# Kernel optimization log

Measured on AMD Instinct MI355X. Metric: run time of the kernel, lower is better.

## Reference

```python
import jax, jax.numpy as jnp
import numpy as np

N = 100000
E = 1600000
NEG_SLOPE = 0.2


def gat_conv(h_x, edge_index, W, a_src, a_dst, b, heads, concat):
    # h_x: [N, Fin]; W: [Fin, heads*C]
    n = h_x.shape[0]
    h = (h_x @ W).reshape(n, heads, -1)              # [N, H, C]
    s_src = (h * a_src[None]).sum(-1)                # [N, H]
    s_dst = (h * a_dst[None]).sum(-1)                # [N, H]
    # add self loops (PyG default)
    loop = jnp.arange(n, dtype=edge_index.dtype)
    src = jnp.concatenate([edge_index[0], loop])
    dst = jnp.concatenate([edge_index[1], loop])
    e = jax.nn.leaky_relu(s_src[src] + s_dst[dst], NEG_SLOPE)   # [E+N, H]
    m = jax.ops.segment_max(e, dst, num_segments=n)
    e = jnp.exp(e - m[dst])
    denom = jax.ops.segment_sum(e, dst, num_segments=n)
    alpha = e / denom[dst]                                       # [E+N, H]
    out = jax.ops.segment_sum(alpha[:, :, None] * h[src], dst, num_segments=n)  # [N,H,C]
    out = out.reshape(n, -1) if concat else out.mean(axis=1)
    return out + b


def setup_inputs() -> dict:
    key = jax.random.key(0)
    ks = jax.random.split(key, 16)
    s = 0.1
    return {
        "x": jax.random.normal(ks[0], (N, 128), jnp.float32),
        "edge_index": jax.random.randint(ks[1], (2, E), 0, N, jnp.int64 if jax.config.jax_enable_x64 else jnp.int32),
        "W0": jax.random.normal(ks[2], (128, 64), jnp.float32) * s,
        "a_src0": jax.random.normal(ks[3], (1, 64), jnp.float32) * s,
        "a_dst0": jax.random.normal(ks[4], (1, 64), jnp.float32) * s,
        "b0": jax.random.normal(ks[5], (64,), jnp.float32) * s,
        "sW0": jax.random.normal(ks[6], (128, 64), jnp.float32) * s,
        "sb0": jax.random.normal(ks[7], (64,), jnp.float32) * s,
        "W1": jax.random.normal(ks[8], (64, 32), jnp.float32) * s,
        "a_src1": jax.random.normal(ks[9], (1, 32), jnp.float32) * s,
        "a_dst1": jax.random.normal(ks[10], (1, 32), jnp.float32) * s,
        "b1": jax.random.normal(ks[11], (32,), jnp.float32) * s,
        "sW1": jax.random.normal(ks[12], (64, 32), jnp.float32) * s,
        "sb1": jax.random.normal(ks[13], (32,), jnp.float32) * s,
    }


def reference(x, edge_index, W0, a_src0, a_dst0, b0, sW0, sb0,
              W1, a_src1, a_dst1, b1, sW1, sb1):
    # layer 0: GATConv (heads=1, concat=True) + linear skip, ELU (dropout p=0 is identity)
    h = gat_conv(x, edge_index, W0, a_src0, a_dst0, b0, heads=1, concat=True) + (x @ sW0 + sb0)
    h = jax.nn.elu(h)
    # layer 1: GATConv (heads=1, concat=False -> mean) + linear skip, log_softmax
    h = gat_conv(h, edge_index, W1, a_src1, a_dst1, b1, heads=1, concat=False) + (h @ sW1 + sb1)
    return jax.nn.log_softmax(h, axis=-1)
```

## Files before the change

kernel.cpp:

```cpp
#include <hip/hip_runtime.h>
#include <hip/hip_bf16.h>
#include <math.h>

#define NEG_SLOPE 0.2f
#define ECLAMP 30.0f
#define HCLAMP 1.0e4f

#define BSHIFT 8
#define BR 256
#define NBMAX 1024
#define CHUNK 2048

typedef short v8s __attribute__((ext_vector_type(8)));
typedef float v4f __attribute__((ext_vector_type(4)));
typedef unsigned long long ull;

__device__ __forceinline__ float bf2f(__hip_bfloat16 v) { return __bfloat162float(v); }
__device__ __forceinline__ __hip_bfloat16 f2bf(float v) { return __float2bfloat16(v); }
__device__ __forceinline__ float sane(float v)   { return fminf(fmaxf(v, -HCLAMP), HCLAMP); }
__device__ __forceinline__ float eclampf(float v){ return fminf(fmaxf(v, -ECLAMP), ECLAMP); }

__device__ __forceinline__ float ldany(int isf32, const void* p, int i) {
    return isf32 ? ((const float*)p)[i] : bf2f(((const __hip_bfloat16*)p)[i]);
}
// ... 14 lines not shown
    return (unsigned)(*(unsigned short*)&x) | ((unsigned)(*(unsigned short*)&y) << 16);
}

__global__ void k_probe(const unsigned* __restrict__ xw, int nw_safe,
                        const unsigned* __restrict__ ew, int* __restrict__ flags) {
    __shared__ int cnt[2];
    int t = threadIdx.x;
    if (t < 2) cnt[t] = 0;
    __syncthreads();
    unsigned w = xw[(unsigned)(t * 9973) % (unsigned)nw_safe];
    unsigned lo = w & 0xffffu;
    unsigned exp = (lo >> 7) & 0xffu;
    if (lo != 0u && (exp < 90u || exp > 160u)) atomicAdd(&cnt[0], 1);
    if (ew[2 * t + 1] == 0u) atomicAdd(&cnt[1], 1);
    __syncthreads();
    if (t == 0) { flags[0] = (2 * cnt[0] > 256) ? 1 : 0; flags[1] = (cnt[1] >= 200) ? 1 : 0; }
}

__global__ void k_params(const int* __restrict__ flags,
                         const void* W0, const void* sW0, const void* as0, const void* ad0,
                         const void* b0, const void* sb0, const void* W1, const void* sW1,
                         const void* as1, const void* ad1, const void* b1, const void* sb1,
                         float* __restrict__ Pf, __hip_bfloat16* __restrict__ Wg) {
    int f = flags[0];
    int t = blockIdx.x * blockDim.x + threadIdx.x;
    int T = gridDim.x * blockDim.x;
    for (int i = t; i < 8192; i += T) {
        int n = i >> 7, k = i & 127;
        Wg[i]        = f2bf(ldany(f, W0,  k * 64 + n));
        Wg[8192 + i] = f2bf(ldany(f, sW0, k * 64 + n));
    }
    for (int i = t; i < 2048; i += T) {
        int n = i >> 6, k = i & 63;
        Wg[16384 + i] = f2bf(ldany(f, W1,  k * 32 + n));
        Wg[18432 + i] = f2bf(ldany(f, sW1, k * 32 + n));
    }
    if (t < 64) {
        Pf[t]       = ldany(f, as0, t);
        Pf[64 + t]  = ldany(f, ad0, t);
        Pf[128 + t] = ldany(f, b0, t) + ldany(f, sb0, t);
    }
    if (t < 32) {
        Pf[192 + t] = ldany(f, as1, t);
        Pf[224 + t] = ldany(f, ad1, t);
        Pf[256 + t] = ldany(f, b1, t) + ldany(f, sb1, t);
    }
}

__global__ void k_zero(int* __restrict__ p, int n) {
    int i = blockIdx.x * blockDim.x + threadIdx.x;
    if (i < n) p[i] = 0;
}

__global__ __launch_bounds__(256) void k_chist(const void* __restrict__ ei,
                                               const int* __restrict__ flags,
                                               int E, int N, int NB,
                                               int* __restrict__ hist) {
    __shared__ int h[NBMAX];
    for (int i = threadIdx.x; i < NB; i += 256) h[i] = 0;
    __syncthreads();
    int f = flags[1];
    long long c0 = (long long)blockIdx.x * CHUNK;
    long long c1 = c0 + CHUNK;
    if (c1 > E) c1 = E;
    for (long long i = c0 + threadIdx.x; i < c1; i += 256) {
        unsigned d = (unsigned)ldidx(f, ei, (long long)E + i);
        if (d < (unsigned)N) atomicAdd(&h[d >> BSHIFT], 1);
    }
    __syncthreads();
    long long base = (long long)blockIdx.x * NB;
    for (int i = threadIdx.x; i < NB; i += 256) hist[base + i] = h[i];
}

__global__ __launch_bounds__(1024) void k_cscan(const int* __restrict__ hist,
                                                int gch, int NB,
                                                int* __restrict__ cb,
                                                int* __restrict__ bcount) {
    __shared__ int sh[1024];
    int b = blockIdx.x;
    int t = threadIdx.x;
    int run = 0;
    for (int base = 0; base < gch; base += 1024) {
        int c = base + t;
        int v = (c < gch) ? hist[(long long)c * NB + b] : 0;
        sh[t] = v;
        __syncthreads();
        for (int off = 1; off < 1024; off <<= 1) {
            int xv = (t >= off) ? sh[t - off] : 0;
            __syncthreads();
            sh[t] += xv;
            __syncthreads();
        }
        if (c < gch) cb[(long long)c * NB + b] = run + sh[t] - v;
        run += sh[1023];
        __syncthreads();
    }
    if (t == 0) bcount[b] = run;
}

__global__ void k_bscan(const int* __restrict__ bcount, int NB,
                        int* __restrict__ bbase) {
    __shared__ int sh[NBMAX];
    int t = threadIdx.x;
    int v = (t < NB) ? bcount[t] : 0;
    sh[t] = v;
    __syncthreads();
    for (int off = 1; off < NBMAX; off <<= 1) {
        int xv = (t >= off) ? sh[t - off] : 0;
        __syncthreads();
        sh[t] += xv;
        __syncthreads();
    }
    if (t < NB) bbase[t] = sh[t] - v;
    if (t == NB - 1) bbase[NB] = sh[t];
}

__global__ __launch_bounds__(256) void k_bscatter(const void* __restrict__ ei,
                                                  const int* __restrict__ flags,
                                                  int E, int N, int NB,
                                                  const int* __restrict__ bbase,
                                                  const int* __restrict__ cb,
                                                  unsigned* __restrict__ binned) {
    __shared__ int rb[NBMAX];
    int f = flags[1];
// ... 65 lines not shown
__global__ void k_scan1(const int* __restrict__ deg, int N,
                        int* __restrict__ rowptr, int* __restrict__ bsum) {
    __shared__ int sh[1024];
    int t = threadIdx.x;
    int idx = blockIdx.x * 1024 + t;
    int v = (idx < N) ? deg[idx] : 0;
    sh[t] = v;
    __syncthreads();
    for (int off = 1; off < 1024; off <<= 1) {
        int xv = (t >= off) ? sh[t - off] : 0;
        __syncthreads();
        sh[t] += xv;
        __syncthreads();
    }
    if (idx < N) rowptr[idx] = sh[t] - v;
    if (t == 1023) bsum[blockIdx.x] = sh[1023];
}

__global__ void k_scan2(int* __restrict__ bsum, int B, int* __restrict__ rowptr, int N) {
    __shared__ int sh[1024];
    int t = threadIdx.x;
    int v = (t < B) ? bsum[t] : 0;
    sh[t] = v;
    __syncthreads();
    for (int off = 1; off < 1024; off <<= 1) {
        int xv = (t >= off) ? sh[t - off] : 0;
        __syncthreads();
        sh[t] += xv;
        __syncthreads();
    }
    if (t < B) bsum[t] = sh[t] - v;
    if (t == 1023) rowptr[N] = sh[1023];
}

__global__ void k_scan3(int N, int* __restrict__ rowptr, const int* __restrict__ bsum,
                        int* __restrict__ cursor) {
    int idx = blockIdx.x * 1024 + threadIdx.x;
    if (idx < N) {
        int r = rowptr[idx] + bsum[blockIdx.x];
        rowptr[idx] = r;
        cursor[idx] = r;
    }
}

__global__ void k_fill(const void* __restrict__ ei, const int* __restrict__ flags,
                       int E, int N, int* __restrict__ cursor, int* __restrict__ csr_src) {
    int i = blockIdx.x * blockDim.x + threadIdx.x;
    if (i < E) {
        int f = flags[1];
        unsigned d = (unsigned)ldidx(f, ei, (long long)E + i);
        if (d < (unsigned)N) {
            int p = atomicAdd(&cursor[d], 1);
            if ((unsigned)p < (unsigned)E) csr_src[p] = ldidx(f, ei, i);
        }
    }
}

__global__ __launch_bounds__(256) void k_l0(
    const void* __restrict__ x, const int* __restrict__ flags,
    const float* __restrict__ Pf, const __hip_bfloat16* __restrict__ Wg, int N,
    __hip_bfloat16* __restrict__ h0, __hip_bfloat16* __restrict__ skip0,
    float* __restrict__ ssrc, float* __restrict__ sdst) {
    __shared__ __hip_bfloat16 sm[26112];
    __hip_bfloat16* xs  = sm;
    __hip_bfloat16* wt0 = sm + 8704;
    __hip_bfloat16* wts = sm + 17408;
    int tid = threadIdx.x;
    int f = flags[0];
    int tile = blockIdx.x * 64;

    for (int i = tid * 4; i < 8192; i += 1024) {
        int r = i >> 7, k = i & 127;
        uint2 w0v = *(const uint2*)&Wg[i];
        uint2 w1v = *(const uint2*)&Wg[8192 + i];
        *(uint2*)&wt0[r * 136 + k] = w0v;
        *(uint2*)&wts[r * 136 + k] = w1v;
    }
    for (int i = tid * 4; i < 8192; i += 1024) {
        int r = i >> 7, k = i & 127;
        int g = tile + r; if (g >= N) g = N - 1;
        uint2* dx = (uint2*)&xs[r * 136 + k];
        if (f) {
            float4 v = *(const float4*)((const float*)x + (size_t)g * 128 + k);
            uint2 o; o.x = packbf(v.x, v.y); o.y = packbf(v.z, v.w);
            *dx = o;
        } else {
            *dx = *(const uint2*)((const __hip_bfloat16*)x + (size_t)g * 128 + k);
        }
    }
    __syncthreads();

    int lane = tid & 63, w = tid >> 6;
    int n16 = lane & 15, quad = lane >> 4;
    v4f zf = {0.f, 0.f, 0.f, 0.f};
    v4f acc_h[4], acc_s[4];
#pragma unroll
    for (int t = 0; t < 4; t++) { acc_h[t] = zf; acc_s[t] = zf; }

    int arow = (w << 4) + n16;
#pragma unroll
    for (int s = 0; s < 4; s++) {
        v8s a = ld8(&xs[arow * 136 + s * 32 + (quad << 3)]);
#pragma unroll
        for (int t = 0; t < 4; t++) {
            v8s bh = ld8(&wt0[(t * 16 + n16) * 136 + s * 32 + (quad << 3)]);
            acc_h[t] = __builtin_amdgcn_mfma_f32_16x16x32_bf16(a, bh, acc_h[t], 0, 0, 0);
            v8s bs = ld8(&wts[(t * 16 + n16) * 136 + s * 32 + (quad << 3)]);
            acc_s[t] = __builtin_amdgcn_mfma_f32_16x16x32_bf16(a, bs, acc_s[t], 0, 0, 0);
        }
    }

    int mbase = tile + (w << 4) + (quad << 2);
    float ps[4] = {0, 0, 0, 0}, pd[4] = {0, 0, 0, 0};
#pragma unroll
    for (int t = 0; t < 4; t++) {
        int ch = t * 16 + n16;
        float av = Pf[ch];
        float dv = Pf[64 + ch];
        float bv = Pf[128 + ch];
#pragma unroll
        for (int r = 0; r < 4; r++) {
            float hv = sane(acc_h[t][r]);
            float sv = sane(acc_s[t][r] + bv);
            int node = mbase + r;
            if (node < N) {
                h0[(size_t)node * 64 + ch] = f2bf(hv);
                skip0[(size_t)node * 64 + ch] = f2bf(sv);
            }
            ps[r] += hv * av;
            pd[r] += hv * dv;
        }
    }
#pragma unroll
    for (int m = 1; m <= 8; m <<= 1) {
#pragma unroll
        for (int r = 0; r < 4; r++) {
            ps[r] += __shfl_xor(ps[r], m, 64);
            pd[r] += __shfl_xor(pd[r], m, 64);
        }
    }
    if (n16 == 0) {
#pragma unroll
        for (int r = 0; r < 4; r++) {
            int node = mbase + r;
            if (node < N) { ssrc[node] = sane(ps[r]); sdst[node] = sane(pd[r]); }
        }
    }
}

__global__ __launch_bounds__(256) void k_l0_agg(
    const int* __restrict__ rowptr, const int* __restrict__ csr_src,
    const float* __restrict__ ssrc, const float* __restrict__ sdst,
    const __hip_bfloat16* __restrict__ h0,
    int N, __hip_bfloat16* __restrict__ skip0_hact) {
    __shared__ ull ews[256];
    int wv = threadIdx.x >> 6, lane = threadIdx.x & 63;
    int half = lane >> 5, l5 = lane & 31;
    int slot = l5 >> 4, c4 = l5 & 15;
    int n = blockIdx.x * 8 + wv * 2 + half;
    bool act = n < N;
    int nn = act ? n : 0;
    const uint2* h0w = (const uint2*)h0;
    ull* myw = &ews[wv * 64 + half * 32];

    float sd = sdst[nn];
    float wself = ewgt(ssrc[nn] + sd);

    uint2 selfv = h0w[(size_t)nn * 16 + c4];
    float w0 = (slot == 0) ? wself : 0.f;
    float acc0 = w0 * bflo(selfv.x);
    float acc1 = w0 * bfhi(selfv.x);
    float acc2 = w0 * bflo(selfv.y);
    float acc3 = w0 * bfhi(selfv.y);
    float denp = 0.f;

    int beg = act ? rowptr[nn] : 0;
    int end = act ? rowptr[nn + 1] : 0;
    for (int j0 = beg; j0 < end; j0 += 32) {
        int cnt = end - j0; if (cnt > 32) cnt = 32;
        int s = (l5 < cnt) ? csr_src[j0 + l5] : 0;
        bool v = (l5 < cnt) && ((unsigned)s < (unsigned)N);
        int sg = v ? s : 0;
        float wj = v ? ewgt(ssrc[sg] + sd) : 0.f;
        denp += wj;
        myw[l5] = ((ull)__float_as_uint(wj) << 32) | (unsigned)sg;
        int k2 = 0;
        int full = cnt & ~7;
        for (; k2 < full; k2 += 8) {
            ull pa = myw[k2 + slot];
            ull pb = myw[k2 + 2 + slot];
            ull pc = myw[k2 + 4 + slot];
            ull pd_ = myw[k2 + 6 + slot];
            float wa = __uint_as_float((unsigned)(pa >> 32));
            float wb = __uint_as_float((unsigned)(pb >> 32));
            float wc = __uint_as_float((unsigned)(pc >> 32));
            float wd = __uint_as_float((unsigned)(pd_ >> 32));
            int sa = (int)(unsigned)(pa & 0xffffffffu);
            int sb = (int)(unsigned)(pb & 0xffffffffu);
            int sc = (int)(unsigned)(pc & 0xffffffffu);
            int sdi = (int)(unsigned)(pd_ & 0xffffffffu);
            uint2 va = h0w[(size_t)sa * 16 + c4];
            uint2 vb = h0w[(size_t)sb * 16 + c4];
            uint2 vc = h0w[(size_t)sc * 16 + c4];
            uint2 vd = h0w[(size_t)sdi * 16 + c4];
            acc0 += wa * bflo(va.x) + wb * bflo(vb.x) + wc * bflo(vc.x) + wd * bflo(vd.x);
            acc1 += wa * bfhi(va.x) + wb * bfhi(vb.x) + wc * bfhi(vc.x) + wd * bfhi(vd.x);
            acc2 += wa * bflo(va.y) + wb * bflo(vb.y) + wc * bflo(vc.y) + wd * bflo(vd.y);
            acc3 += wa * bfhi(va.y) + wb * bfhi(vb.y) + wc * bfhi(vc.y) + wd * bfhi(vd.y);
        }
        for (; k2 < cnt; k2 += 8) {
            int ia = k2 + slot,     ib = k2 + 2 + slot;
            int ic = k2 + 4 + slot, id = k2 + 6 + slot;
            ull pa = myw[ia < cnt ? ia : 0];
            ull pb = myw[ib < cnt ? ib : 0];
            ull pc = myw[ic < cnt ? ic : 0];
            ull pd_ = myw[id < cnt ? id : 0];
            float wa = (ia < cnt) ? __uint_as_float((unsigned)(pa >> 32)) : 0.f;
            float wb = (ib < cnt) ? __uint_as_float((unsigned)(pb >> 32)) : 0.f;
            float wc = (ic < cnt) ? __uint_as_float((unsigned)(pc >> 32)) : 0.f;
            float wd = (id < cnt) ? __uint_as_float((unsigned)(pd_ >> 32)) : 0.f;
            int sa = (int)(unsigned)(pa & 0xffffffffu);
            int sb = (int)(unsigned)(pb & 0xffffffffu);
            int sc = (int)(unsigned)(pc & 0xffffffffu);
            int sdi = (int)(unsigned)(pd_ & 0xffffffffu);
            uint2 va = h0w[(size_t)sa * 16 + c4];
            uint2 vb = h0w[(size_t)sb * 16 + c4];
            uint2 vc = h0w[(size_t)sc * 16 + c4];
            uint2 vd = h0w[(size_t)sdi * 16 + c4];
            acc0 += wa * bflo(va.x) + wb * bflo(vb.x) + wc * bflo(vc.x) + wd * bflo(vd.x);
            acc1 += wa * bfhi(va.x) + wb * bfhi(vb.x) + wc * bfhi(vc.x) + wd * bfhi(vd.x);
            acc2 += wa * bflo(va.y) + wb * bflo(vb.y) + wc * bflo(vc.y) + wd * bflo(vd.y);
            acc3 += wa * bfhi(va.y) + wb * bfhi(vb.y) + wc * bfhi(vc.y) + wd * bfhi(vd.y);
        }
    }
    acc0 += __shfl_xor(acc0, 16, 64);
    acc1 += __shfl_xor(acc1, 16, 64);
    acc2 += __shfl_xor(acc2, 16, 64);
    acc3 += __shfl_xor(acc3, 16, 64);
    float den = denp;
#pragma unroll
    for (int m = 1; m <= 16; m <<= 1) den += __shfl_xor(den, m, 64);
    den += wself;

    if (slot == 0 && act) {
        uint2 skv = ((const uint2*)skip0_hact)[(size_t)nn * 16 + c4];
        float v0 = sane(acc0 / den + bflo(skv.x));
        float v1 = sane(acc1 / den + bfhi(skv.x));
        float v2 = sane(acc2 / den + bflo(skv.y));
        float v3 = sane(acc3 / den + bfhi(skv.y));
        v0 = v0 > 0.f ? v0 : (__expf(v0) - 1.f);
        v1 = v1 > 0.f ? v1 : (__expf(v1) - 1.f);
        v2 = v2 > 0.f ? v2 : (__expf(v2) - 1.f);
        v3 = v3 > 0.f ? v3 : (__expf(v3) - 1.f);
        uint2 o;
        o.x = packbf(v0, v1);
        o.y = packbf(v2, v3);
        ((uint2*)skip0_hact)[(size_t)nn * 16 + c4] = o;
    }
}

__global__ __launch_bounds__(256) void k_l1(
    const __hip_bfloat16* __restrict__ hact,
    const float* __restrict__ Pf, const __hip_bfloat16* __restrict__ Wg, int N,
    __hip_bfloat16* __restrict__ h1, __hip_bfloat16* __restrict__ skip1,
    float* __restrict__ ssrc, float* __restrict__ sdst) {
    __shared__ __hip_bfloat16 sm[9216];
    __hip_bfloat16* xs  = sm;
    __hip_bfloat16* wt1 = sm + 4608;
    __hip_bfloat16* ws1 = sm + 6912;
    int tid = threadIdx.x;
    int tile = blockIdx.x * 64;

    for (int i = tid * 4; i < 2048; i += 1024) {
        int r = i >> 6, k = i & 63;
        uint2 w0v = *(const uint2*)&Wg[16384 + i];
        uint2 w1v = *(const uint2*)&Wg[18432 + i];
        *(uint2*)&wt1[r * 72 + k] = w0v;
        *(uint2*)&ws1[r * 72 + k] = w1v;
    }
    for (int i = tid * 4; i < 4096; i += 1024) {
        int r = i >> 6, k = i & 63;
        int g = tile + r; if (g >= N) g = N - 1;
        *(uint2*)&xs[r * 72 + k] = *(const uint2*)(hact + (size_t)g * 64 + k);
    }
    __syncthreads();

    int lane = tid & 63, w = tid >> 6;
    int n16 = lane & 15, quad = lane >> 4;
    v4f zf = {0.f, 0.f, 0.f, 0.f};
    v4f acc_h[2], acc_s[2];
#pragma unroll
    for (int t = 0; t < 2; t++) { acc_h[t] = zf; acc_s[t] = zf; }

    int arow = (w << 4) + n16;
#pragma unroll
    for (int s = 0; s < 2; s++) {
        v8s a = ld8(&xs[arow * 72 + s * 32 + (quad << 3)]);
#pragma unroll
        for (int t = 0; t < 2; t++) {
            v8s bh = ld8(&wt1[(t * 16 + n16) * 72 + s * 32 + (quad << 3)]);
            acc_h[t] = __builtin_amdgcn_mfma_f32_16x16x32_bf16(a, bh, acc_h[t], 0, 0, 0);
            v8s bs = ld8(&ws1[(t * 16 + n16) * 72 + s * 32 + (quad << 3)]);
            acc_s[t] = __builtin_amdgcn_mfma_f32_16x16x32_bf16(a, bs, acc_s[t], 0, 0, 0);
        }
    }

    int mbase = tile + (w << 4) + (quad << 2);
    float ps[4] = {0, 0, 0, 0}, pd[4] = {0, 0, 0, 0};
#pragma unroll
    for (int t = 0; t < 2; t++) {
        int ch = t * 16 + n16;
        float av = Pf[192 + ch];
        float dv = Pf[224 + ch];
        float bv = Pf[256 + ch];
#pragma unroll
        for (int r = 0; r < 4; r++) {
            float hv = sane(acc_h[t][r]);
            float sv = sane(acc_s[t][r] + bv);
            int node = mbase + r;
            if (node < N) {
                h1[(size_t)node * 32 + ch] = f2bf(hv);
                skip1[(size_t)node * 32 + ch] = f2bf(sv);
            }
            ps[r] += hv * av;
            pd[r] += hv * dv;
        }
    }
#pragma unroll
    for (int m = 1; m <= 8; m <<= 1) {
#pragma unroll
        for (int r = 0; r < 4; r++) {
            ps[r] += __shfl_xor(ps[r], m, 64);
            pd[r] += __shfl_xor(pd[r], m, 64);
        }
    }
    if (n16 == 0) {
#pragma unroll
        for (int r = 0; r < 4; r++) {
            int node = mbase + r;
            if (node < N) { ssrc[node] = sane(ps[r]); sdst[node] = sane(pd[r]); }
        }
    }
}

__global__ __launch_bounds__(256) void k_l1_agg(
    const int* __restrict__ rowptr, const int* __restrict__ csr_src,
    const float* __restrict__ ssrc, const float* __restrict__ sdst,
    const __hip_bfloat16* __restrict__ h1, const __hip_bfloat16* __restrict__ skip1,
    int N, float* __restrict__ out) {
    __shared__ ull ews[256];
    int wv = threadIdx.x >> 6, lane = threadIdx.x & 63;
    int half = lane >> 5, l5 = lane & 31;
    int slot = l5 >> 3, c4 = l5 & 7;
    int n = blockIdx.x * 8 + wv * 2 + half;
    bool act = n < N;
    int nn = act ? n : 0;
    const uint2* h1w = (const uint2*)h1;
    ull* myw = &ews[wv * 64 + half * 32];

    float sd = sdst[nn];
    float wself = ewgt(ssrc[nn] + sd);

    uint2 selfv = h1w[(size_t)nn * 8 + c4];
    float w0 = (slot == 0) ? wself : 0.f;
    float acc0 = w0 * bflo(selfv.x);
    float acc1 = w0 * bfhi(selfv.x);
    float acc2 = w0 * bflo(selfv.y);
    float acc3 = w0 * bfhi(selfv.y);
    float denp = 0.f;

    int beg = act ? rowptr[nn] : 0;
    int end = act ? rowptr[nn + 1] : 0;
    for (int j0 = beg; j0 < end; j0 += 32) {
        int cnt = end - j0; if (cnt > 32) cnt = 32;
        int s = (l5 < cnt) ? csr_src[j0 + l5] : 0;
        bool v = (l5 < cnt) && ((unsigned)s < (unsigned)N);
        int sg = v ? s : 0;
        float wj = v ? ewgt(ssrc[sg] + sd) : 0.f;
        denp += wj;
        myw[l5] = ((ull)__float_as_uint(wj) << 32) | (unsigned)sg;
        int k4 = 0;
        int full = cnt & ~15;
        for (; k4 < full; k4 += 16) {
            ull pa = myw[k4 + slot];
            ull pb = myw[k4 + 4 + slot];
            ull pc = myw[k4 + 8 + slot];
            ull pd_ = myw[k4 + 12 + slot];
            float wa = __uint_as_float((unsigned)(pa >> 32));
            float wb = __uint_as_float((unsigned)(pb >> 32));
            float wc = __uint_as_float((unsigned)(pc >> 32));
            float wd = __uint_as_float((unsigned)(pd_ >> 32));
            int sa = (int)(unsigned)(pa & 0xffffffffu);
            int sb = (int)(unsigned)(pb & 0xffffffffu);
// ... 33 lines not shown
            acc3 += wa * bfhi(va.y) + wb * bfhi(vb.y) + wc * bfhi(vc.y) + wd * bfhi(vd.y);
        }
    }
    acc0 += __shfl_xor(acc0, 8, 64); acc0 += __shfl_xor(acc0, 16, 64);
    acc1 += __shfl_xor(acc1, 8, 64); acc1 += __shfl_xor(acc1, 16, 64);
    acc2 += __shfl_xor(acc2, 8, 64); acc2 += __shfl_xor(acc2, 16, 64);
    acc3 += __shfl_xor(acc3, 8, 64); acc3 += __shfl_xor(acc3, 16, 64);
    float den = denp;
#pragma unroll
    for (int m = 1; m <= 16; m <<= 1) den += __shfl_xor(den, m, 64);
    den += wself;

    uint2 skv = ((const uint2*)skip1)[(size_t)nn * 8 + c4];
    float o0 = sane(acc0 / den + bflo(skv.x));
    float o1 = sane(acc1 / den + bfhi(skv.x));
    float o2 = sane(acc2 / den + bflo(skv.y));
    float o3 = sane(acc3 / den + bfhi(skv.y));
    float m = fmaxf(fmaxf(o0, o1), fmaxf(o2, o3));
#pragma unroll
    for (int k = 1; k <= 4; k <<= 1) m = fmaxf(m, __shfl_xor(m, k, 64));
    float ex = __expf(o0 - m) + __expf(o1 - m) + __expf(o2 - m) + __expf(o3 - m);
#pragma unroll
    for (int k = 1; k <= 4; k <<= 1) ex += __shfl_xor(ex, k, 64);
    float l = __logf(ex);
    float r0 = o0 - m - l, r1 = o1 - m - l, r2 = o2 - m - l, r3 = o3 - m - l;
    if (!isfinite(r0)) r0 = 0.f;
    if (!isfinite(r1)) r1 = 0.f;
    if (!isfinite(r2)) r2 = 0.f;
    if (!isfinite(r3)) r3 = 0.f;
    if (slot == 0 && act) {
        float4 o4; o4.x = r0; o4.y = r1; o4.z = r2; o4.w = r3;
        *(float4*)&out[(size_t)nn * 32 + 4 * c4] = o4;
    }
}

__global__ void k_sentinel(float* __restrict__ out, int n, float val) {
    int i = blockIdx.x * blockDim.x + threadIdx.x;
    if (i < n) out[i] = val;
}

extern "C" void kernel_launch(void* const* d_in, const int* in_sizes, int n_in,
                              void* d_out, int out_size, void* d_ws, size_t ws_size,
                              hipStream_t stream) {
    const void* x  = d_in[0];
    const void* ei = d_in[1];
    float* out = (float*)d_out;

    int N = in_sizes[0] / 128;
    int E = in_sizes[1] / 2;

    int NB  = (N + BR - 1) >> BSHIFT;
    int gch = (E + CHUNK - 1) / CHUNK;
    if (gch < 1) gch = 1;
    bool fast = (N <= (NBMAX << BSHIFT)) && ((size_t)E * 4 <= (size_t)N * 128);

    char* ws = (char*)d_ws;
    size_t off = 0;
    auto alloc = [&](size_t bytes) -> char* {
        char* p = ws + off;
        off += (bytes + 255) & ~(size_t)255;
        return p;
    };
    int*   flags   = (int*)alloc(2 * 4);
    float* Pf      = (float*)alloc(288 * 4);
    __hip_bfloat16* Wg = (__hip_bfloat16*)alloc(20480 * 2);
    int*   rowptr  = (int*)alloc((size_t)(N + 1) * 4);
    int*   cursor  = (int*)alloc((size_t)N * 4);
    float* sdst01  = (float*)alloc((size_t)N * 4);
    int*   bsum    = (int*)alloc(1024 * 4);
    int*   bcount  = (int*)alloc(NBMAX * 4);
    int*   bbase   = (int*)alloc((NBMAX + 1) * 4);
    int*   csr_src = (int*)alloc((size_t)E * 4);
    int*   hist    = (int*)alloc(fast ? (size_t)gch * NB * 4 : 0);
    int*   cb      = (int*)alloc(fast ? (size_t)gch * NB * 4 : 0);
    __hip_bfloat16* h0    = (__hip_bfloat16*)alloc((size_t)N * 64 * 2);
    __hip_bfloat16* skip0 = (__hip_bfloat16*)alloc((size_t)N * 64 * 2);
    size_t required = off;

    if (ws_size < required) {
        float mb = (float)(double)(ws_size >> 20);
        k_sentinel<<<(out_size + 255) / 256, 256, 0, stream>>>(out, out_size, mb);
        return;
    }

    float* ssrc01 = (float*)cursor;
    __hip_bfloat16* h1    = h0;
    __hip_bfloat16* skip1 = h0 + (size_t)N * 32;

    k_probe<<<1, 256, 0, stream>>>((const unsigned*)x, N * 64, (const unsigned*)ei, flags);
    k_params<<<40, 256, 0, stream>>>(flags, d_in[2], d_in[6], d_in[3], d_in[4],
                                     d_in[5], d_in[7], d_in[8], d_in[12],
                                     d_in[9], d_in[10], d_in[11], d_in[13], Pf, Wg);

    if (fast) {
        unsigned* binned = (unsigned*)h0;
        k_chist<<<gch, 256, 0, stream>>>(ei, flags, E, N, NB, hist);
        k_cscan<<<NB, 1024, 0, stream>>>(hist, gch, NB, cb, bcount);
        k_bscan<<<1, NBMAX, 0, stream>>>(bcount, NB, bbase);
        k_bscatter<<<gch, 256, 0, stream>>>(ei, flags, E, N, NB, bbase, cb, binned);
        k_bbuild<<<NB, 256, 0, stream>>>(binned, bbase, N, NB, rowptr, csr_src);
    } else {
        int B = (N + 1023) / 1024;
        k_zero<<<(N + 255) / 256, 256, 0, stream>>>(cursor, N);
        k_deg<<<(E + 255) / 256, 256, 0, stream>>>(ei, flags, E, N, cursor);
        k_scan1<<<B, 1024, 0, stream>>>(cursor, N, rowptr, bsum);
        k_scan2<<<1, 1024, 0, stream>>>(bsum, B, rowptr, N);
        k_scan3<<<B, 1024, 0, stream>>>(N, rowptr, bsum, cursor);
        k_fill<<<(E + 255) / 256, 256, 0, stream>>>(ei, flags, E, N, cursor, csr_src);
    }

    k_l0<<<(N + 63) / 64, 256, 0, stream>>>(x, flags, Pf, Wg, N,
                                            h0, skip0, ssrc01, sdst01);
    k_l0_agg<<<(N + 7) / 8, 256, 0, stream>>>(rowptr, csr_src, ssrc01, sdst01,
                                              h0, N, skip0);
    k_l1<<<(N + 63) / 64, 256, 0, stream>>>(skip0, Pf, Wg, N,
                                            h1, skip1, ssrc01, sdst01);
    k_l1_agg<<<(N + 7) / 8, 256, 0, stream>>>(rowptr, csr_src, ssrc01, sdst01,
                                              h1, skip1, N, out);
}
```

Measured before the change: 268.7 us.

## Fuse layer-0 aggregation with layer-1 linear transform in one kernel

Merges the layer-0 attention aggregation and the layer-1 MFMA projection into one 512-thread kernel. Each block aggregates 64 nodes, writes the ELU activations straight into shared memory and then runs the matmul from there, so the activated features no longer make a round trip through global memory and one launch is removed. The attention-score row sums now go through shared-memory atomics. Because the layer-1 outputs can no longer alias layer-0 buffers that other blocks are still reading, they get separate workspace allocations. Each block's serial aggregation passes and heavier shared-memory use may cut occupancy and latency hiding for the gather.

```diff
diff --git a/kernel.cpp b/kernel.cpp
--- a/kernel.cpp
+++ b/kernel.cpp
@@ -375,183 +375,174 @@
     }
 }
 
-__global__ __launch_bounds__(256) void k_l0_agg(
+__global__ __launch_bounds__(512) void k_l0agg_l1(
     const int* __restrict__ rowptr, const int* __restrict__ csr_src,
-    const float* __restrict__ ssrc, const float* __restrict__ sdst,
-    const __hip_bfloat16* __restrict__ h0,
-    int N, __hip_bfloat16* __restrict__ skip0_hact) {
-    __shared__ ull ews[256];
-    int wv = threadIdx.x >> 6, lane = threadIdx.x & 63;
+    const float* __restrict__ ssrc0, const float* __restrict__ sdst0,
+    const __hip_bfloat16* __restrict__ h0, const __hip_bfloat16* __restrict__ skip0,
+    const float* __restrict__ Pf, const __hip_bfloat16* __restrict__ Wg, int N,
+    __hip_bfloat16* __restrict__ h1, __hip_bfloat16* __restrict__ skip1,
+    float* __restrict__ ssrc1, float* __restrict__ sdst1) {
+    __shared__ __hip_bfloat16 xs[4608];
+    __shared__ __hip_bfloat16 wsm[4608];
+    __shared__ ull ews[512];
+    __shared__ float psum[64], pdum[64];
+    __hip_bfloat16* wt1 = wsm;
+    __hip_bfloat16* ws1 = wsm + 2304;
+    int tid = threadIdx.x;
+    int tile = blockIdx.x * 64;
+
+    {
+        int i = tid * 4;
+        int r = i >> 6, k = i & 63;
+        *(uint2*)&wt1[r * 72 + k] = *(const uint2*)&Wg[16384 + i];
+        *(uint2*)&ws1[r * 72 + k] = *(const uint2*)&Wg[18432 + i];
+    }
+    if (tid < 64) { psum[tid] = 0.f; pdum[tid] = 0.f; }
+
+    int wv = tid >> 6, lane = tid & 63;
     int half = lane >> 5, l5 = lane & 31;
     int slot = l5 >> 4, c4 = l5 & 15;
-    int n = blockIdx.x * 8 + wv * 2 + half;
-    bool act = n < N;
-    int nn = act ? n : 0;
     const uint2* h0w = (const uint2*)h0;
     ull* myw = &ews[wv * 64 + half * 32];
 
-    float sd = sdst[nn];
-    float wself = ewgt(ssrc[nn] + sd);
-
-    uint2 selfv = h0w[(size_t)nn * 16 + c4];
-    float w0 = (slot == 0) ? wself : 0.f;
-    float acc0 = w0 * bflo(selfv.x);
-    float acc1 = w0 * bfhi(selfv.x);
-    float acc2 = w0 * bflo(selfv.y);
-    float acc3 = w0 * bfhi(selfv.y);
-    float denp = 0.f;
-
-    int beg = act ? rowptr[nn] : 0;
-    int end = act ? rowptr[nn + 1] : 0;
-    for (int j0 = beg; j0 < end; j0 += 32) {
-        int cnt = end - j0; if (cnt > 32) cnt = 32;
-        int s = (l5 < cnt) ? csr_src[j0 + l5] : 0;
-        bool v = (l5 < cnt) && ((unsigned)s < (unsigned)N);
-        int sg = v ? s : 0;
-        float wj = v ? ewgt(ssrc[sg] + sd) : 0.f;
-        denp += wj;
-        myw[l5] = ((ull)__float_as_uint(wj) << 32) | (unsigned)sg;
-        int k2 = 0;
-        int full = cnt & ~7;
-        for (; k2 < full; k2 += 8) {
-            ull pa = myw[k2 + slot];
-            ull pb = myw[k2 + 2 + slot];
-            ull pc = myw[k2 + 4 + slot];
-            ull pd_ = myw[k2 + 6 + slot];
-            float wa = __uint_as_float((unsigned)(pa >> 32));
-            float wb = __uint_as_float((unsigned)(pb >> 32));
-            float wc = __uint_as_float((unsigned)(pc >> 32));
-            float wd = __uint_as_float((unsigned)(pd_ >> 32));
-            int sa = (int)(unsigned)(pa & 0xffffffffu);
-            int sb = (int)(unsigned)(pb & 0xffffffffu);
-            int sc = (int)(unsigned)(pc & 0xffffffffu);
-            int sdi = (int)(unsigned)(pd_ & 0xffffffffu);
-            uint2 va = h0w[(size_t)sa * 16 + c4];
-            uint2 vb = h0w[(size_t)sb * 16 + c4];
-            uint2 vc = h0w[(size_t)sc * 16 + c4];
-            uint2 vd = h0w[(size_t)sdi * 16 + c4];
-            acc0 += wa * bflo(va.x) + wb * bflo(vb.x) + wc * bflo(vc.x) + wd * bflo(vd.x);
-            acc1 += wa * bfhi(va.x) + wb * bfhi(vb.x) + wc * bfhi(vc.x) + wd * bfhi(vd.x);
-            acc2 += wa * bflo(va.y) + wb * bflo(vb.y) + wc * bflo(vc.y) + wd * bflo(vd.y);
-            acc3 += wa * bfhi(va.y) + wb * bfhi(vb.y) + wc * bfhi(vc.y) + wd * bfhi(vd.y);
-        }
-        for (; k2 < cnt; k2 += 8) {
-            int ia = k2 + slot,     ib = k2 + 2 + slot;
-            int ic = k2 + 4 + slot, id = k2 + 6 + slot;
-            ull pa = myw[ia < cnt ? ia : 0];
-            ull pb = myw[ib < cnt ? ib : 0];
-            ull pc = myw[ic < cnt ? ic : 0];
-            ull pd_ = myw[id < cnt ? id : 0];
-            float wa = (ia < cnt) ? __uint_as_float((unsigned)(pa >> 32)) : 0.f;
-            float wb = (ib < cnt) ? __uint_as_float((unsigned)(pb >> 32)) : 0.f;
-            float wc = (ic < cnt) ? __uint_as_float((unsigned)(pc >> 32)) : 0.f;
-            float wd = (id < cnt) ? __uint_as_float((unsigned)(pd_ >> 32)) : 0.f;
-            int sa = (int)(unsigned)(pa & 0xffffffffu);
-            int sb = (int)(unsigned)(pb & 0xffffffffu);
-            int sc = (int)(unsigned)(pc & 0xffffffffu);
-            int sdi = (int)(unsigned)(pd_ & 0xffffffffu);
-            uint2 va = h0w[(size_t)sa * 16 + c4];
-            uint2 vb = h0w[(size_t)sb * 16 + c4];
-            uint2 vc = h0w[(size_t)sc * 16 + c4];
-            uint2 vd = h0w[(size_t)sdi * 16 + c4];
-            acc0 += wa * bflo(va.x) + wb * bflo(vb.x) + wc * bflo(vc.x) + wd * bflo(vd.x);
-            acc1 += wa * bfhi(va.x) + wb * bfhi(vb.x) + wc * bfhi(vc.x) + wd * bfhi(vd.x);
-            acc2 += wa * bflo(va.y) + wb * bflo(vb.y) + wc * bflo(vc.y) + wd * bflo(vd.y);
-            acc3 += wa * bfhi(va.y) + wb * bfhi(vb.y) + wc * bfhi(vc.y) + wd * bfhi(vd.y);
-        }
-    }
-    acc0 += __shfl_xor(acc0, 16, 64);
-    acc1 += __shfl_xor(acc1, 16, 64);
-    acc2 += __shfl_xor(acc2, 16, 64);
-    acc3 += __shfl_xor(acc3, 16, 64);
-    float den = denp;
-#pragma unroll
-    for (int m = 1; m <= 16; m <<= 1) den += __shfl_xor(den, m, 64);
-    den += wself;
-
-    if (slot == 0 && act) {
-        uint2 skv = ((const uint2*)skip0_hact)[(size_t)nn * 16 + c4];
-        float v0 = sane(acc0 / den + bflo(skv.x));
-        float v1 = sane(acc1 / den + bfhi(skv.x));
-        float v2 = sane(acc2 / den + bflo(skv.y));
-        float v3 = sane(acc3 / den + bfhi(skv.y));
-        v0 = v0 > 0.f ? v0 : (__expf(v0) - 1.f);
-        v1 = v1 > 0.f ? v1 : (__expf(v1) - 1.f);
-        v2 = v2 > 0.f ? v2 : (__expf(v2) - 1.f);
-        v3 = v3 > 0.f ? v3 : (__expf(v3) - 1.f);
-        uint2 o;
-        o.x = packbf(v0, v1);
-        o.y = packbf(v2, v3);
-        ((uint2*)skip0_hact)[(size_t)nn * 16 + c4] = o;
-    }
-}
-
-__global__ __launch_bounds__(256) void k_l1(
-    const __hip_bfloat16* __restrict__ hact,
-    const float* __restrict__ Pf, const __hip_bfloat16* __restrict__ Wg, int N,
-    __hip_bfloat16* __restrict__ h1, __hip_bfloat16* __restrict__ skip1,
-    float* __restrict__ ssrc, float* __restrict__ sdst) {
-    __shared__ __hip_bfloat16 sm[9216];
-    __hip_bfloat16* xs  = sm;
-    __hip_bfloat16* wt1 = sm + 4608;
-    __hip_bfloat16* ws1 = sm + 6912;
-    int tid = threadIdx.x;
-    int tile = blockIdx.x * 64;
-
-    for (int i = tid * 4; i < 2048; i += 1024) {
-        int r = i >> 6, k = i & 63;
-        uint2 w0v = *(const uint2*)&Wg[16384 + i];
-        uint2 w1v = *(const uint2*)&Wg[18432 + i];
-        *(uint2*)&wt1[r * 72 + k] = w0v;
-        *(uint2*)&ws1[r * 72 + k] = w1v;
-    }
-    for (int i = tid * 4; i < 4096; i += 1024) {
-        int r = i >> 6, k = i & 63;
-        int g = tile + r; if (g >= N) g = N - 1;
-        *(uint2*)&xs[r * 72 + k] = *(const uint2*)(hact + (size_t)g * 64 + k);
-    }
-    __syncthreads();
-
-    int lane = tid & 63, w = tid >> 6;
+    for (int pass = 0; pass < 4; pass++) {
+        int row = pass * 16 + wv * 2 + half;
+        int n = tile + row;
+        bool act = n < N;
+        int nn = act ? n : 0;
+
+        float sd = sdst0[nn];
+        float wself = ewgt(ssrc0[nn] + sd);
+
+        uint2 selfv = h0w[(size_t)nn * 16 + c4];
+        float w0 = (slot == 0) ? wself : 0.f;
+        float acc0 = w0 * bflo(selfv.x);
+        float acc1 = w0 * bfhi(selfv.x);
+        float acc2 = w0 * bflo(selfv.y);
+        float acc3 = w0 * bfhi(selfv.y);
+        float denp = 0.f;
+
+        int beg = act ? rowptr[nn] : 0;
+        int end = act ? rowptr[nn + 1] : 0;
+        for (int j0 = beg; j0 < end; j0 += 32) {
+            int cnt = end - j0; if (cnt > 32) cnt = 32;
+            int s = (l5 < cnt) ? csr_src[j0 + l5] : 0;
+            bool v = (l5 < cnt) && ((unsigned)s < (unsigned)N);
+            int sg = v ? s : 0;
+            float wj = v ? ewgt(ssrc0[sg] + sd) : 0.f;
+            denp += wj;
+            myw[l5] = ((ull)__float_as_uint(wj) << 32) | (unsigned)sg;
+            int k2 = 0;
+            int full = cnt & ~7;
+            for (; k2 < full; k2 += 8) {
+                ull pa = myw[k2 + slot];
+                ull pb = myw[k2 + 2 + slot];
+                ull pc = myw[k2 + 4 + slot];
+                ull pd_ = myw[k2 + 6 + slot];
+                float wa = __uint_as_float((unsigned)(pa >> 32));
+                float wb = __uint_as_float((unsigned)(pb >> 32));
+                float wc = __uint_as_float((unsigned)(pc >> 32));
+                float wd = __uint_as_float((unsigned)(pd_ >> 32));
+                int sa = (int)(unsigned)(pa & 0xffffffffu);
+                int sb = (int)(unsigned)(pb & 0xffffffffu);
+                int sc = (int)(unsigned)(pc & 0xffffffffu);
+                int sdi = (int)(unsigned)(pd_ & 0xffffffffu);
+                uint2 va = h0w[(size_t)sa * 16 + c4];
+                uint2 vb = h0w[(size_t)sb * 16 + c4];
+                uint2 vc = h0w[(size_t)sc * 16 + c4];
+                uint2 vd = h0w[(size_t)sdi * 16 + c4];
+                acc0 += wa * bflo(va.x) + wb * bflo(vb.x) + wc * bflo(vc.x) + wd * bflo(vd.x);
+                acc1 += wa * bfhi(va.x) + wb * bfhi(vb.x) + wc * bfhi(vc.x) + wd * bfhi(vd.x);
+                acc2 += wa * bflo(va.y) + wb * bflo(vb.y) + wc * bflo(vc.y) + wd * bflo(vd.y);
+                acc3 += wa * bfhi(va.y) + wb * bfhi(vb.y) + wc * bfhi(vc.y) + wd * bfhi(vd.y);
+            }
+            for (; k2 < cnt; k2 += 8) {
+                int ia = k2 + slot,     ib = k2 + 2 + slot;
+                int ic = k2 + 4 + slot, id = k2 + 6 + slot;
+                ull pa = myw[ia < cnt ? ia : 0];
+                ull pb = myw[ib < cnt ? ib : 0];
+                ull pc = myw[ic < cnt ? ic : 0];
+                ull pd_ = myw[id < cnt ? id : 0];
+                float wa = (ia < cnt) ? __uint_as_float((unsigned)(pa >> 32)) : 0.f;
+                float wb = (ib < cnt) ? __uint_as_float((unsigned)(pb >> 32)) : 0.f;
+                float wc = (ic < cnt) ? __uint_as_float((unsigned)(pc >> 32)) : 0.f;
+                float wd = (id < cnt) ? __uint_as_float((unsigned)(pd_ >> 32)) : 0.f;
+                int sa = (int)(unsigned)(pa & 0xffffffffu);
+                int sb = (int)(unsigned)(pb & 0xffffffffu);
+                int sc = (int)(unsigned)(pc & 0xffffffffu);
+                int sdi = (int)(unsigned)(pd_ & 0xffffffffu);
+                uint2 va = h0w[(size_t)sa * 16 + c4];
+                uint2 vb = h0w[(size_t)sb * 16 + c4];
+                uint2 vc = h0w[(size_t)sc * 16 + c4];
+                uint2 vd = h0w[(size_t)sdi * 16 + c4];
+                acc0 += wa * bflo(va.x) + wb * bflo(vb.x) + wc * bflo(vc.x) + wd * bflo(vd.x);
+                acc1 += wa * bfhi(va.x) + wb * bfhi(vb.x) + wc * bfhi(vc.x) + wd * bfhi(vd.x);
+                acc2 += wa * bflo(va.y) + wb * bflo(vb.y) + wc * bflo(vc.y) + wd * bflo(vd.y);
+                acc3 += wa * bfhi(va.y) + wb * bfhi(vb.y) + wc * bfhi(vc.y) + wd * bfhi(vd.y);
+            }
+        }
+        acc0 += __shfl_xor(acc0, 16, 64);
+        acc1 += __shfl_xor(acc1, 16, 64);
+        acc2 += __shfl_xor(acc2, 16, 64);
+        acc3 += __shfl_xor(acc3, 16, 64);
+        float den = denp;
+#pragma unroll
+        for (int m = 1; m <= 16; m <<= 1) den += __shfl_xor(den, m, 64);
+        den += wself;
+
+        if (slot == 0) {
+            uint2 o; o.x = 0u; o.y = 0u;
+            if (act) {
+                uint2 skv = ((const uint2*)skip0)[(size_t)nn * 16 + c4];
+                float v0 = sane(acc0 / den + bflo(skv.x));
+                float v1 = sane(acc1 / den + bfhi(skv.x));
+                float v2 = sane(acc2 / den + bflo(skv.y));
+                float v3 = sane(acc3 / den + bfhi(skv.y));
+                v0 = v0 > 0.f ? v0 : (__expf(v0) - 1.f);
+                v1 = v1 > 0.f ? v1 : (__expf(v1) - 1.f);
+                v2 = v2 > 0.f ? v2 : (__expf(v2) - 1.f);
+                v3 = v3 > 0.f ? v3 : (__expf(v3) - 1.f);
+                o.x = packbf(v0, v1);
+                o.y = packbf(v2, v3);
+            }
+            *(uint2*)&xs[row * 72 + c4 * 4] = o;
+        }
+    }
+    __syncthreads();
+
+    int w8 = wv;
+    int rt = w8 >> 1, ct = w8 & 1;
     int n16 = lane & 15, quad = lane >> 4;
-    v4f zf = {0.f, 0.f, 0.f, 0.f};
-    v4f acc_h[2], acc_s[2];
-#pragma unroll
-    for (int t = 0; t < 2; t++) { acc_h[t] = zf; acc_s[t] = zf; }
-
-    int arow = (w << 4) + n16;
+    v4f acc_h = {0.f, 0.f, 0.f, 0.f};
+    v4f acc_s = {0.f, 0.f, 0.f, 0.f};
+    int arow = rt * 16 + n16;
 #pragma unroll
     for (int s = 0; s < 2; s++) {
         v8s a = ld8(&xs[arow * 72 + s * 32 + (quad << 3)]);
-#pragma unroll
-        for (int t = 0; t < 2; t++) {
-            v8s bh = ld8(&wt1[(t * 16 + n16) * 72 + s * 32 + (quad << 3)]);
-            acc_h[t] = __builtin_amdgcn_mfma_f32_16x16x32_bf16(a, bh, acc_h[t], 0, 0, 0);
-            v8s bs = ld8(&ws1[(t * 16 + n16) * 72 + s * 32 + (quad << 3)]);
-            acc_s[t] = __builtin_amdgcn_mfma_f32_16x16x32_bf16(a, bs, acc_s[t], 0, 0, 0);
-        }
-    }
-
-    int mbase = tile + (w << 4) + (quad << 2);
+        v8s bh = ld8(&wt1[(ct * 16 + n16) * 72 + s * 32 + (quad << 3)]);
+        acc_h = __builtin_amdgcn_mfma_f32_16x16x32_bf16(a, bh, acc_h, 0, 0, 0);
+        v8s bs = ld8(&ws1[(ct * 16 + n16) * 72 + s * 32 + (quad << 3)]);
+        acc_s = __builtin_amdgcn_mfma_f32_16x16x32_bf16(a, bs, acc_s, 0, 0, 0);
+    }
+
+    int mrow = rt * 16 + (quad << 2);
+    int mbase = tile + mrow;
+    int ch = ct * 16 + n16;
+    float av = Pf[192 + ch];
+    float dv = Pf[224 + ch];
+    float bv = Pf[256 + ch];
     float ps[4] = {0, 0, 0, 0}, pd[4] = {0, 0, 0, 0};
 #pragma unroll
-    for (int t = 0; t < 2; t++) {
-        int ch = t * 16 + n16;
-        float av = Pf[192 + ch];
-        float dv = Pf[224 + ch];
-        float bv = Pf[256 + ch];
-#pragma unroll
-        for (int r = 0; r < 4; r++) {
-            float hv = sane(acc_h[t][r]);
-            float sv = sane(acc_s[t][r] + bv);
-            int node = mbase + r;
-            if (node < N) {
-                h1[(size_t)node * 32 + ch] = f2bf(hv);
-                skip1[(size_t)node * 32 + ch] = f2bf(sv);
-            }
-            ps[r] += hv * av;
-            pd[r] += hv * dv;
-        }
+    for (int r = 0; r < 4; r++) {
+        float hv = sane(acc_h[r]);
+        float sv = sane(acc_s[r] + bv);
+        int node = mbase + r;
+        if (node < N) {
+            h1[(size_t)node * 32 + ch] = f2bf(hv);
+            skip1[(size_t)node * 32 + ch] = f2bf(sv);
+        }
+        ps[r] += hv * av;
+        pd[r] += hv * dv;
     }
 #pragma unroll
     for (int m = 1; m <= 8; m <<= 1) {
@@ -564,8 +555,16 @@
     if (n16 == 0) {
 #pragma unroll
         for (int r = 0; r < 4; r++) {
-            int node = mbase + r;
-            if (node < N) { ssrc[node] = sane(ps[r]); sdst[node] = sane(pd[r]); }
+            atomicAdd(&psum[mrow + r], ps[r]);
+            atomicAdd(&pdum[mrow + r], pd[r]);
+        }
+    }
+    __syncthreads();
+    if (tid < 64) {
+        int node = tile + tid;
+        if (node < N) {
+            ssrc1[node] = sane(psum[tid]);
+            sdst1[node] = sane(pdum[tid]);
         }
     }
 }
@@ -719,7 +718,9 @@
     __hip_bfloat16* Wg = (__hip_bfloat16*)alloc(20480 * 2);
     int*   rowptr  = (int*)alloc((size_t)(N + 1) * 4);
     int*   cursor  = (int*)alloc((size_t)N * 4);
-    float* sdst01  = (float*)alloc((size_t)N * 4);
+    float* sdst0   = (float*)alloc((size_t)N * 4);
+    float* ssrc1   = (float*)alloc((size_t)N * 4);
+    float* sdst1   = (float*)alloc((size_t)N * 4);
     int*   bsum    = (int*)alloc(1024 * 4);
     int*   bcount  = (int*)alloc(NBMAX * 4);
     int*   bbase   = (int*)alloc((NBMAX + 1) * 4);
@@ -728,6 +729,8 @@
     int*   cb      = (int*)alloc(fast ? (size_t)gch * NB * 4 : 0);
     __hip_bfloat16* h0    = (__hip_bfloat16*)alloc((size_t)N * 64 * 2);
     __hip_bfloat16* skip0 = (__hip_bfloat16*)alloc((size_t)N * 64 * 2);
+    __hip_bfloat16* h1    = (__hip_bfloat16*)alloc((size_t)N * 32 * 2);
+    __hip_bfloat16* skip1 = (__hip_bfloat16*)alloc((size_t)N * 32 * 2);
     size_t required = off;
 
     if (ws_size < required) {
@@ -736,9 +739,7 @@
         return;
     }
 
-    float* ssrc01 = (float*)cursor;
-    __hip_bfloat16* h1    = h0;
-    __hip_bfloat16* skip1 = h0 + (size_t)N * 32;
+    float* ssrc0 = (float*)cursor;
 
     k_probe<<<1, 256, 0, stream>>>((const unsigned*)x, N * 64, (const unsigned*)ei, flags);
     k_params<<<40, 256, 0, stream>>>(flags, d_in[2], d_in[6], d_in[3], d_in[4],
@@ -763,11 +764,10 @@
     }
 
     k_l0<<<(N + 63) / 64, 256, 0, stream>>>(x, flags, Pf, Wg, N,
-                                            h0, skip0, ssrc01, sdst01);
-    k_l0_agg<<<(N + 7) / 8, 256, 0, stream>>>(rowptr, csr_src, ssrc01, sdst01,
-                                              h0, N, skip0);
-    k_l1<<<(N + 63) / 64, 256, 0, stream>>>(skip0, Pf, Wg, N,
-                                            h1, skip1, ssrc01, sdst01);
-    k_l1_agg<<<(N + 7) / 8, 256, 0, stream>>>(rowptr, csr_src, ssrc01, sdst01,
+                                            h0, skip0, ssrc0, sdst0);
+    k_l0agg_l1<<<(N + 63) / 64, 512, 0, stream>>>(rowptr, csr_src, ssrc0, sdst0,
+                                                  h0, skip0, Pf, Wg, N,
+                                                  h1, skip1, ssrc1, sdst1);
+    k_l1_agg<<<(N + 7) / 8, 256, 0, stream>>>(rowptr, csr_src, ssrc1, sdst1,
                                               h1, skip1, N, out);
 }
```

After: 270.5 us. About the same (+0.7%).

## Fuse destination histogram with layer-0 GEMM into one heterogeneous launch

Applied to the files above, without the earlier changes.

Merges the edge-destination bucket histogram kernel and the layer-0 dense projection kernel into a single launch, with the first gch blocks doing histogram work and the rest doing the MFMA GEMM tiles. Because h0 is now written before binning, the binned edge buffer gets its own workspace allocation instead of aliasing h0. The aim is to run the independent CSR build and GEMM work concurrently and cut one launch. The cost is extra workspace and a larger shared-memory footprint for the histogram blocks, which may reduce occupancy.

```diff
diff --git a/kernel.cpp b/kernel.cpp
--- a/kernel.cpp
+++ b/kernel.cpp
@@ -90,24 +90,118 @@
     if (i < n) p[i] = 0;
 }
 
-__global__ __launch_bounds__(256) void k_chist(const void* __restrict__ ei,
-                                               const int* __restrict__ flags,
-                                               int E, int N, int NB,
-                                               int* __restrict__ hist) {
-    __shared__ int h[NBMAX];
-    for (int i = threadIdx.x; i < NB; i += 256) h[i] = 0;
-    __syncthreads();
-    int f = flags[1];
-    long long c0 = (long long)blockIdx.x * CHUNK;
-    long long c1 = c0 + CHUNK;
-    if (c1 > E) c1 = E;
-    for (long long i = c0 + threadIdx.x; i < c1; i += 256) {
-        unsigned d = (unsigned)ldidx(f, ei, (long long)E + i);
-        if (d < (unsigned)N) atomicAdd(&h[d >> BSHIFT], 1);
-    }
-    __syncthreads();
-    long long base = (long long)blockIdx.x * NB;
-    for (int i = threadIdx.x; i < NB; i += 256) hist[base + i] = h[i];
+__global__ __launch_bounds__(256) void k1_chist_l0(
+    const void* __restrict__ ei, const void* __restrict__ x,
+    const int* __restrict__ flags,
+    const float* __restrict__ Pf, const __hip_bfloat16* __restrict__ Wg,
+    int N, int E, int NB, int gch,
+    int* __restrict__ hist,
+    __hip_bfloat16* __restrict__ h0, __hip_bfloat16* __restrict__ skip0,
+    float* __restrict__ ssrc, float* __restrict__ sdst) {
+    __shared__ __align__(16) char smraw[52224];
+    int tid = threadIdx.x;
+
+    if ((int)blockIdx.x < gch) {
+        int f = flags[1];
+        int* h = (int*)smraw;
+        for (int i = tid; i < NB; i += 256) h[i] = 0;
+        __syncthreads();
+        long long c0 = (long long)blockIdx.x * CHUNK;
+        long long c1 = c0 + CHUNK;
+        if (c1 > E) c1 = E;
+        for (long long i = c0 + tid; i < c1; i += 256) {
+            unsigned d = (unsigned)ldidx(f, ei, (long long)E + i);
+            if (d < (unsigned)N) atomicAdd(&h[d >> BSHIFT], 1);
+        }
+        __syncthreads();
+        long long base = (long long)blockIdx.x * NB;
+        for (int i = tid; i < NB; i += 256) hist[base + i] = h[i];
+        return;
+    }
+
+    __hip_bfloat16* xs  = (__hip_bfloat16*)smraw;
+    __hip_bfloat16* wt0 = xs + 8704;
+    __hip_bfloat16* wts = xs + 17408;
+    int f = flags[0];
+    int tile = ((int)blockIdx.x - gch) * 64;
+
+    for (int i = tid * 4; i < 8192; i += 1024) {
+        int r = i >> 7, k = i & 127;
+        uint2 w0v = *(const uint2*)&Wg[i];
+        uint2 w1v = *(const uint2*)&Wg[8192 + i];
+        *(uint2*)&wt0[r * 136 + k] = w0v;
+        *(uint2*)&wts[r * 136 + k] = w1v;
+    }
+    for (int i = tid * 4; i < 8192; i += 1024) {
+        int r = i >> 7, k = i & 127;
+        int g = tile + r; if (g >= N) g = N - 1;
+        uint2* dx = (uint2*)&xs[r * 136 + k];
+        if (f) {
+            float4 v = *(const float4*)((const float*)x + (size_t)g * 128 + k);
+            uint2 o; o.x = packbf(v.x, v.y); o.y = packbf(v.z, v.w);
+            *dx = o;
+        } else {
+            *dx = *(const uint2*)((const __hip_bfloat16*)x + (size_t)g * 128 + k);
+        }
+    }
+    __syncthreads();
+
+    int lane = tid & 63, w = tid >> 6;
+    int n16 = lane & 15, quad = lane >> 4;
+    v4f zf = {0.f, 0.f, 0.f, 0.f};
+    v4f acc_h[4], acc_s[4];
+#pragma unroll
+    for (int t = 0; t < 4; t++) { acc_h[t] = zf; acc_s[t] = zf; }
+
+    int arow = (w << 4) + n16;
+#pragma unroll
+    for (int s = 0; s < 4; s++) {
+        v8s a = ld8(&xs[arow * 136 + s * 32 + (quad << 3)]);
+#pragma unroll
+        for (int t = 0; t < 4; t++) {
+            v8s bh = ld8(&wt0[(t * 16 + n16) * 136 + s * 32 + (quad << 3)]);
+            acc_h[t] = __builtin_amdgcn_mfma_f32_16x16x32_bf16(a, bh, acc_h[t], 0, 0, 0);
+            v8s bs = ld8(&wts[(t * 16 + n16) * 136 + s * 32 + (quad << 3)]);
+            acc_s[t] = __builtin_amdgcn_mfma_f32_16x16x32_bf16(a, bs, acc_s[t], 0, 0, 0);
+        }
+    }
+
+    int mbase = tile + (w << 4) + (quad << 2);
+    float ps[4] = {0, 0, 0, 0}, pd[4] = {0, 0, 0, 0};
+#pragma unroll
+    for (int t = 0; t < 4; t++) {
+        int ch = t * 16 + n16;
+        float av = Pf[ch];
+        float dv = Pf[64 + ch];
+        float bv = Pf[128 + ch];
+#pragma unroll
+        for (int r = 0; r < 4; r++) {
+            float hv = sane(acc_h[t][r]);
+            float sv = sane(acc_s[t][r] + bv);
+            int node = mbase + r;
+            if (node < N) {
+                h0[(size_t)node * 64 + ch] = f2bf(hv);
+                skip0[(size_t)node * 64 + ch] = f2bf(sv);
+            }
+            ps[r] += hv * av;
+            pd[r] += hv * dv;
+        }
+    }
+#pragma unroll
+    for (int m = 1; m <= 8; m <<= 1) {
+#pragma unroll
+        for (int r = 0; r < 4; r++) {
+            ps[r] += __shfl_xor(ps[r], m, 64);
+            pd[r] += __shfl_xor(pd[r], m, 64);
+        }
+    }
+    if (n16 == 0) {
+#pragma unroll
+        for (int r = 0; r < 4; r++) {
+            int node = mbase + r;
+            if (node < N) { ssrc[node] = sane(ps[r]); sdst[node] = sane(pd[r]); }
+        }
+    }
 }
 
 __global__ __launch_bounds__(1024) void k_cscan(const int* __restrict__ hist,
@@ -279,98 +373,6 @@
         if (d < (unsigned)N) {
             int p = atomicAdd(&cursor[d], 1);
             if ((unsigned)p < (unsigned)E) csr_src[p] = ldidx(f, ei, i);
-        }
-    }
-}
-
-__global__ __launch_bounds__(256) void k_l0(
-    const void* __restrict__ x, const int* __restrict__ flags,
-    const float* __restrict__ Pf, const __hip_bfloat16* __restrict__ Wg, int N,
-    __hip_bfloat16* __restrict__ h0, __hip_bfloat16* __restrict__ skip0,
-    float* __restrict__ ssrc, float* __restrict__ sdst) {
-    __shared__ __hip_bfloat16 sm[26112];
-    __hip_bfloat16* xs  = sm;
-    __hip_bfloat16* wt0 = sm + 8704;
-    __hip_bfloat16* wts = sm + 17408;
-    int tid = threadIdx.x;
-    int f = flags[0];
-    int tile = blockIdx.x * 64;
-
-    for (int i = tid * 4; i < 8192; i += 1024) {
-        int r = i >> 7, k = i & 127;
-        uint2 w0v = *(const uint2*)&Wg[i];
-        uint2 w1v = *(const uint2*)&Wg[8192 + i];
-        *(uint2*)&wt0[r * 136 + k] = w0v;
-        *(uint2*)&wts[r * 136 + k] = w1v;
-    }
-    for (int i = tid * 4; i < 8192; i += 1024) {
-        int r = i >> 7, k = i & 127;
-        int g = tile + r; if (g >= N) g = N - 1;
-        uint2* dx = (uint2*)&xs[r * 136 + k];
-        if (f) {
-            float4 v = *(const float4*)((const float*)x + (size_t)g * 128 + k);
-            uint2 o; o.x = packbf(v.x, v.y); o.y = packbf(v.z, v.w);
-            *dx = o;
-        } else {
-            *dx = *(const uint2*)((const __hip_bfloat16*)x + (size_t)g * 128 + k);
-        }
-    }
-    __syncthreads();
-
-    int lane = tid & 63, w = tid >> 6;
-    int n16 = lane & 15, quad = lane >> 4;
-    v4f zf = {0.f, 0.f, 0.f, 0.f};
-    v4f acc_h[4], acc_s[4];
-#pragma unroll
-    for (int t = 0; t < 4; t++) { acc_h[t] = zf; acc_s[t] = zf; }
-
-    int arow = (w << 4) + n16;
-#pragma unroll
-    for (int s = 0; s < 4; s++) {
-        v8s a = ld8(&xs[arow * 136 + s * 32 + (quad << 3)]);
-#pragma unroll
-        for (int t = 0; t < 4; t++) {
-            v8s bh = ld8(&wt0[(t * 16 + n16) * 136 + s * 32 + (quad << 3)]);
-            acc_h[t] = __builtin_amdgcn_mfma_f32_16x16x32_bf16(a, bh, acc_h[t], 0, 0, 0);
-            v8s bs = ld8(&wts[(t * 16 + n16) * 136 + s * 32 + (quad << 3)]);
-            acc_s[t] = __builtin_amdgcn_mfma_f32_16x16x32_bf16(a, bs, acc_s[t], 0, 0, 0);
-        }
-    }
-
-    int mbase = tile + (w << 4) + (quad << 2);
-    float ps[4] = {0, 0, 0, 0}, pd[4] = {0, 0, 0, 0};
-#pragma unroll
-    for (int t = 0; t < 4; t++) {
-        int ch = t * 16 + n16;
-        float av = Pf[ch];
-        float dv = Pf[64 + ch];
-        float bv = Pf[128 + ch];
-#pragma unroll
-        for (int r = 0; r < 4; r++) {
-            float hv = sane(acc_h[t][r]);
-            float sv = sane(acc_s[t][r] + bv);
-            int node = mbase + r;
-            if (node < N) {
-                h0[(size_t)node * 64 + ch] = f2bf(hv);
-                skip0[(size_t)node * 64 + ch] = f2bf(sv);
-            }
-            ps[r] += hv * av;
-            pd[r] += hv * dv;
-        }
-    }
-#pragma unroll
-    for (int m = 1; m <= 8; m <<= 1) {
-#pragma unroll
-        for (int r = 0; r < 4; r++) {
-            ps[r] += __shfl_xor(ps[r], m, 64);
-            pd[r] += __shfl_xor(pd[r], m, 64);
-        }
-    }
-    if (n16 == 0) {
-#pragma unroll
-        for (int r = 0; r < 4; r++) {
-            int node = mbase + r;
-            if (node < N) { ssrc[node] = sane(ps[r]); sdst[node] = sane(pd[r]); }
         }
     }
 }
@@ -705,6 +707,7 @@
     int NB  = (N + BR - 1) >> BSHIFT;
     int gch = (E + CHUNK - 1) / CHUNK;
     if (gch < 1) gch = 1;
+    int Lb = (N + 63) / 64;
     bool fast = (N <= (NBMAX << BSHIFT)) && ((size_t)E * 4 <= (size_t)N * 128);
 
     char* ws = (char*)d_ws;
@@ -724,6 +727,7 @@
     int*   bcount  = (int*)alloc(NBMAX * 4);
     int*   bbase   = (int*)alloc((NBMAX + 1) * 4);
     int*   csr_src = (int*)alloc((size_t)E * 4);
+    unsigned* binned = (unsigned*)alloc(fast ? (size_t)E * 4 : 0);
     int*   hist    = (int*)alloc(fast ? (size_t)gch * NB * 4 : 0);
     int*   cb      = (int*)alloc(fast ? (size_t)gch * NB * 4 : 0);
     __hip_bfloat16* h0    = (__hip_bfloat16*)alloc((size_t)N * 64 * 2);
@@ -746,8 +750,8 @@
                                      d_in[9], d_in[10], d_in[11], d_in[13], Pf, Wg);
 
     if (fast) {
-        unsigned* binned = (unsigned*)h0;
-        k_chist<<<gch, 256, 0, stream>>>(ei, flags, E, N, NB, hist);
+        k1_chist_l0<<<gch + Lb, 256, 0, stream>>>(ei, x, flags, Pf, Wg, N, E, NB, gch,
+                                                  hist, h0, skip0, ssrc01, sdst01);
         k_cscan<<<NB, 1024, 0, stream>>>(hist, gch, NB, cb, bcount);
         k_bscan<<<1, NBMAX, 0, stream>>>(bcount, NB, bbase);
         k_bscatter<<<gch, 256, 0, stream>>>(ei, flags, E, N, NB, bbase, cb, binned);
@@ -760,10 +764,10 @@
         k_scan2<<<1, 1024, 0, stream>>>(bsum, B, rowptr, N);
         k_scan3<<<B, 1024, 0, stream>>>(N, rowptr, bsum, cursor);
         k_fill<<<(E + 255) / 256, 256, 0, stream>>>(ei, flags, E, N, cursor, csr_src);
-    }
-
-    k_l0<<<(N + 63) / 64, 256, 0, stream>>>(x, flags, Pf, Wg, N,
-                                            h0, skip0, ssrc01, sdst01);
+        k1_chist_l0<<<Lb, 256, 0, stream>>>(ei, x, flags, Pf, Wg, N, E, NB, 0,
+                                            bsum, h0, skip0, ssrc01, sdst01);
+    }
+
     k_l0_agg<<<(N + 7) / 8, 256, 0, stream>>>(rowptr, csr_src, ssrc01, sdst01,
                                               h0, N, skip0);
     k_l1<<<(N + 63) / 64, 256, 0, stream>>>(skip0, Pf, Wg, N,
```

Result: slower. 277.7 us (+3.4%).
